# Performance work log

Measured on AMD Instinct MI355X. Metric: run time of the kernel, lower is better.

## Reference

```python
import jax, jax.numpy as jnp
import numpy as np

B, N, C, H = 2, 128, 256, 8
D = C // H
SCALE = D ** -0.5
LN_EPS = 1e-5


def _layernorm(x, g, b):
    mu = jnp.mean(x, axis=-1, keepdims=True)
    var = jnp.mean((x - mu) ** 2, axis=-1, keepdims=True)
    return (x - mu) * jax.lax.rsqrt(var + LN_EPS) * g + b


def setup_inputs() -> dict:
    key = jax.random.key(0)
    ks = jax.random.split(key, 12)
    s = 0.02
    return {
        "e": jax.random.normal(ks[0], (B, N, N, C), jnp.float32),
        "mask": jnp.zeros((B, N, N, H), jnp.float32),
        "ln_g": jnp.ones((C,), jnp.float32),
        "ln_b": jnp.zeros((C,), jnp.float32),
        "W_qkv_in": jax.random.normal(ks[1], (C, 3 * C), jnp.float32) * s,
        "b_qkv_in": jnp.zeros((3 * C,), jnp.float32),
        "W_E_in": jax.random.normal(ks[2], (C, H), jnp.float32) * s,
        "b_E_in": jnp.zeros((H,), jnp.float32),
        "W_qkv_out": jax.random.normal(ks[3], (C, 3 * C), jnp.float32) * s,
        "b_qkv_out": jnp.zeros((3 * C,), jnp.float32),
        "W_E_out": jax.random.normal(ks[4], (C, H), jnp.float32) * s,
        "b_E_out": jnp.zeros((H,), jnp.float32),
        "W_O": jax.random.normal(ks[5], (2 * C, C), jnp.float32) * s,
        "b_O": jnp.zeros((C,), jnp.float32),
    }


def reference(e, mask, ln_g, ln_b, W_qkv_in, b_qkv_in, W_E_in, b_E_in,
              W_qkv_out, b_qkv_out, W_E_out, b_E_out, W_O, b_O):
    b_, n, _, c = e.shape
    e_ln = _layernorm(e, ln_g, ln_b)

    def qkv(W, bias):
        z = e_ln @ W + bias  # [B,N,N,3C]
        q, k, v = jnp.split(z, 3, axis=-1)
        rs = lambda t: t.reshape(b_, n, n, D, H)
        return rs(q) * SCALE, rs(k), rs(v)

    # --- in pass ---
    Q, K, V = qkv(W_qkv_in, b_qkv_in)
    E_in = (e_ln @ W_E_in + b_E_in)[:, :, None, :, :]       # [B,N,1,N,H]
    H_in = jnp.einsum('bijdh,bjkdh->bijkh', Q, K) + E_in
    A_in = jax.nn.softmax(H_in + mask[:, :, None, :, :], axis=3)
    Va_in = jnp.einsum('bijkh,bjkdh->bijdh', A_in, V)

    # --- out pass ---
    Q, K, V = qkv(W_qkv_out, b_qkv_out)
    E_out = (e_ln @ W_E_out + b_E_out)[:, :, :, None, :]    # [B,N,N,1,H]
    H_out = jnp.einsum('bijdh,bkjdh->bkijh', Q, K) + E_out
    A_out = jax.nn.softmax(H_out + mask[:, :, :, None, :], axis=1)
    Va_out = jnp.einsum('bkijh,bkjdh->bijdh', A_out, V)

    Va = jnp.concatenate([Va_in, Va_out], axis=-1).reshape(b_, n, n, 2 * c)
    return Va @ W_O + b_O
```

## Files before the change

kernel.cpp:

```cpp
#include <hip/hip_runtime.h>

typedef unsigned short u16;
typedef __attribute__((ext_vector_type(8))) short bf16x8;
typedef __attribute__((ext_vector_type(4))) float f32x4;

#define SCALE 0.17677669529663687f

__device__ __forceinline__ float us2f(u16 u){ return __uint_as_float(((unsigned int)u)<<16); }
__device__ __forceinline__ u16 f2us(float f){
  unsigned int x = __float_as_uint(f);
  x += 0x7fffu + ((x>>16)&1u);
  return (u16)(x>>16);
}
__device__ __forceinline__ void gl_lds16(const u16* g, u16* l){
  __builtin_amdgcn_global_load_lds(
    (const __attribute__((address_space(1))) unsigned int*)g,
    (__attribute__((address_space(3))) unsigned int*)l, 16, 0, 0);
}

__global__ __launch_bounds__(256) void ln_prep(const float* __restrict__ e, const float* __restrict__ g,
                                               const float* __restrict__ bb, u16* __restrict__ eln,
                                               const float* __restrict__ Wi, const float* __restrict__ WEi,
                                               const float* __restrict__ Wo, const float* __restrict__ WEo,
                                               const float* __restrict__ WO,
                                               u16* __restrict__ WtI, u16* __restrict__ WtO,
                                               u16* __restrict__ WOt){
  int bid = blockIdx.x;
  int t = threadIdx.x;
  if (bid < 8192){
    int tok = bid*4 + (t>>6);
    int lane = t & 63;
    int c0 = lane*4;
    float4 x = *(const float4*)(e + tok*256 + c0);
    float sum = x.x+x.y+x.z+x.w;
    float sq  = x.x*x.x + x.y*x.y + x.z*x.z + x.w*x.w;
    #pragma unroll
    for (int off=32; off>=1; off>>=1){ sum += __shfl_xor(sum, off); sq += __shfl_xor(sq, off); }
    float mu = sum * 0.00390625f;
    float var = sq * 0.00390625f - mu*mu;
    float rstd = rsqrtf(var + 1e-5f);
    float4 gv = *(const float4*)(g + c0);
    float4 bv = *(const float4*)(bb + c0);
    ushort4 o;
    o.x = f2us((x.x-mu)*rstd*gv.x + bv.x);
    o.y = f2us((x.y-mu)*rstd*gv.y + bv.y);
    o.z = f2us((x.z-mu)*rstd*gv.z + bv.z);
    o.w = f2us((x.w-mu)*rstd*gv.w + bv.w);
    *(ushort4*)(eln + tok*256 + c0) = o;
  } else {
    int idx = (bid - 8192)*256 + t;
    if (idx < 425984){
      int which = idx >= 212992;
      int id2 = which ? idx - 212992 : idx;
      const float* W  = which ? Wo  : Wi;
      const float* WE = which ? WEo : WEi;
      u16* Wt = which ? WtO : WtI;
      int n = id2 >> 8, k = id2 & 255;
      float v;
      if (n < 768){
        int sec = n >> 8, r = n & 255, h = r >> 5, d = r & 31;
        v = W[k*768 + sec*256 + d*8 + h];
      } else if (n < 776) v = WE[k*8 + (n-768)];
      else v = 0.f;
      Wt[id2] = f2us(v);
    } else if (idx < 557056){
      int id2 = idx - 425984;
      int n = id2 >> 9, kp = id2 & 511;
      int pass = kp >> 8, h = (kp >> 5) & 7, d = kp & 31;
      int r = d*16 + pass*8 + h;
      WOt[id2] = f2us(WO[r*256 + n]);
    }
  }
}

__global__ __launch_bounds__(256) void qkv_gemm(const u16* __restrict__ eln, const u16* __restrict__ Wt,
    const float* __restrict__ bqkv, const float* __restrict__ bE, const float* __restrict__ mask,
    u16* __restrict__ Qb, u16* __restrict__ Kb, u16* __restrict__ Vb, u16* __restrict__ biasP,
    int pass){
  __shared__ __align__(16) u16 smem[24576];
  int t = threadIdx.x;
  int g = blockIdx.x >> 8;
  int tmb = blockIdx.x & 255;
  int row0 = tmb*128, col0 = g*64;
  int w = t >> 6, lane = t & 63, quad = lane >> 4, l15 = lane & 15;
  int lr = lane >> 3, cc = lane & 7;
  int sw8 = (cc ^ lr) << 3;

  u16* A0 = smem;          u16* A1 = smem + 8192;
  u16* B0 = smem + 16384;  u16* B1 = smem + 20480;

  auto STAGE = [&](int kc, u16* Ab, u16* Bb){
    #pragma unroll
    for (int i=0; i<4; ++i){
      int lrow = w*32 + i*8;
      gl_lds16(eln + (row0 + lrow + lr)*256 + kc*64 + sw8, &Ab[lrow*64]);
    }
    #pragma unroll
    for (int j=0; j<2; ++j){
      int brow = w*16 + j*8;
      gl_lds16(Wt + (col0 + brow + lr)*256 + kc*64 + sw8, &Bb[brow*64]);
    }
  };

  f32x4 zero = {0.f,0.f,0.f,0.f};
  f32x4 acc[2][4];
  #pragma unroll
  for (int mt=0; mt<2; ++mt)
    #pragma unroll
    for (int nt=0; nt<4; ++nt) acc[mt][nt] = zero;

  STAGE(0, A0, B0);
  STAGE(1, A1, B1);

  #pragma unroll
  for (int kc=0; kc<4; ++kc){
    if (kc == 3) { asm volatile("s_waitcnt vmcnt(0)" ::: "memory"); }
    else         { asm volatile("s_waitcnt vmcnt(6)" ::: "memory"); }
    __builtin_amdgcn_s_barrier();
    __builtin_amdgcn_sched_barrier(0);
    u16* Ac = (kc&1) ? A1 : A0;
    u16* Bc = (kc&1) ? B1 : B0;
    #pragma unroll
    for (int s=0; s<2; ++s){
      bf16x8 aF[2], bF[4];
      #pragma unroll
      for (int mt=0; mt<2; ++mt){
        int row = w*32 + mt*16 + l15;
        aF[mt] = *(const bf16x8*)&Ac[row*64 + ((((s<<2)+quad) ^ (l15&7))<<3)];
      }
      #pragma unroll
      for (int nt=0; nt<4; ++nt){
        int row = nt*16 + l15;
        bF[nt] = *(const bf16x8*)&Bc[row*64 + ((((s<<2)+quad) ^ (l15&7))<<3)];
      }
      #pragma unroll
      for (int mt=0; mt<2; ++mt)
        #pragma unroll
        for (int nt=0; nt<4; ++nt)
          acc[mt][nt] = __builtin_amdgcn_mfma_f32_16x16x32_bf16(aF[mt], bF[nt], acc[mt][nt], 0,0,0);
    }
    __builtin_amdgcn_sched_barrier(0);
    __builtin_amdgcn_s_barrier();
    __builtin_amdgcn_sched_barrier(0);
    if (kc < 2) STAGE(kc+2, Ac, Bc);
  }

  if (g < 12){
    int sec = g >> 2;
    float scl = (sec == 0) ? SCALE : 1.0f;
    u16* OutT = smem;
    #pragma unroll
    for (int mt=0; mt<2; ++mt){
      #pragma unroll
      for (int nt=0; nt<4; ++nt){
        int col = col0 + nt*16 + l15;
        int r = col & 255;
        float bias = bqkv[sec*256 + (r&31)*8 + (r>>5)];
        #pragma unroll
        for (int rr=0; rr<4; ++rr){
          int row = w*32 + mt*16 + quad*4 + rr;
          OutT[row*72 + nt*16 + l15] = f2us((acc[mt][nt][rr] + bias) * scl);
        }
      }
    }
    __syncthreads();
    u16* dst = (sec==0) ? Qb : (sec==1) ? Kb : Vb;
    int tr = (sec==0) || pass;
    int bq = tmb >> 7, iq = tmb & 127;
    int rbase = col0 & 255;
    int rrow = t >> 3, rc8 = (t & 7) * 8;
    #pragma unroll
    for (int k=0; k<4; ++k){
      int row = k*32 + rrow;
      uint4 v4 = *(const uint4*)&OutT[row*72 + rc8];
      int tok = tr ? (bq*16384 + row*128 + iq) : (row0 + row);
      *(uint4*)(dst + tok*256 + rbase + rc8) = v4;
    }
  } else {
    if (l15 < 8){
      int h = l15;
      #pragma unroll
      for (int mt=0; mt<2; ++mt){
        #pragma unroll
        for (int rr=0; rr<4; ++rr){
          int tok = row0 + w*32 + mt*16 + quad*4 + rr;
          float v = acc[mt][0][rr];
          int bb = tok >> 14, t1 = (tok >> 7) & 127, t2 = tok & 127;
          int tq = pass ? t2 : t1, tk = pass ? t1 : t2;
          float bv2 = v + bE[h] + mask[tok*8 + h];
          biasP[(((bb*8 + h)*128 + tq)*128) + (tk & 15)*8 + (tk >> 4)] = f2us(bv2);
        }
      }
    }
  }
}

__global__ __launch_bounds__(256) void attn_mfma(const u16* __restrict__ Qb, const u16* __restrict__ Kb,
    const u16* __restrict__ Vb, const u16* __restrict__ biasP, u16* __restrict__ Va, int pass){
  __shared__ __align__(16) u16 uni[16384];
  __shared__ __align__(16) u16 VsT[32][128];
  typedef u16 row40[40];
  typedef u16 row128[128];
  row40*  Qs = (row40*)uni;
  row40*  Ks = (row40*)(uni + 5120);
  row128* Ps = (row128*)uni;
  int t = threadIdx.x;
  int bx = blockIdx.x;
  int h = bx & 7, j = (bx>>3) & 127, b = bx >> 10;

  int base = ((b*128 + j)*128)*256 + h*32;
  #pragma unroll
  for (int it2=0; it2<2; ++it2){
    int idx = it2*256 + t;
    int row = idx >> 2, seg = idx & 3;
    int off = base + row*256 + seg*8;
    *(uint4*)&Qs[row][seg*8] = *(const uint4*)(Qb + off);
    *(uint4*)&Ks[row][seg*8] = *(const uint4*)(Kb + off);
    uint4 vv = *(const uint4*)(Vb + off);
    const u16* vp = (const u16*)&vv;
    #pragma unroll
    for (int q=0;q<8;++q){
      int d = seg*8 + q;
      VsT[d][((((row>>3) ^ q) & 15) << 3) | (row & 7)] = vp[q];
    }
  }
  __syncthreads();

  int w = t >> 6, lane = t & 63, quad = lane >> 4, l15 = lane & 15;
  bf16x8 aQ[2];
  #pragma unroll
  for (int it=0; it<2; ++it) aQ[it] = *(const bf16x8*)&Qs[w*32 + it*16 + l15][quad*8];
  f32x4 zero = {0.f,0.f,0.f,0.f};
  f32x4 S[2][8];
  #pragma unroll
  for (int tk=0; tk<8; ++tk){
    bf16x8 bK = *(const bf16x8*)&Ks[tk*16 + l15][quad*8];
    #pragma unroll
    for (int it=0; it<2; ++it)
      S[it][tk] = __builtin_amdgcn_mfma_f32_16x16x32_bf16(aQ[it], bK, zero, 0,0,0);
  }
  __syncthreads();
  const u16* bpP = biasP + ((b*8 + h)*128)*128;
  float inv[2][4];
  #pragma unroll
  for (int it=0; it<2; ++it){
    #pragma unroll
    for (int r=0; r<4; ++r){
      int i = w*32 + it*16 + quad*4 + r;
      uint4 b4 = *(const uint4*)(bpP + i*128 + l15*8);
      const u16* bu = (const u16*)&b4;
      float l = 0.f;
      float sv[8];
      #pragma unroll
      for (int tk=0; tk<8; ++tk){
        float p = __expf(S[it][tk][r] + us2f(bu[tk]));
        sv[tk] = p; l += p;
      }
      l += __shfl_xor(l,1); l += __shfl_xor(l,2); l += __shfl_xor(l,4); l += __shfl_xor(l,8);
      inv[it][r] = 1.0f / l;
      #pragma unroll
      for (int tk=0; tk<8; ++tk)
        Ps[i][(((tk*2 + (l15>>3)) ^ (i&7)) << 3) | (l15&7)] = f2us(sv[tk]);
    }
  }
  f32x4 O[2][2];
  #pragma unroll
  for (int it=0; it<2; ++it)
    #pragma unroll
    for (int dt=0; dt<2; ++dt) O[it][dt] = zero;
  #pragma unroll
  for (int kc=0; kc<4; ++kc){
    bf16x8 bV[2];
    #pragma unroll
    for (int dt=0; dt<2; ++dt)
      bV[dt] = *(const bf16x8*)&VsT[dt*16 + l15][(((kc*4 + quad) ^ (l15&7)) & 15) << 3];
    #pragma unroll
    for (int it=0; it<2; ++it){
      bf16x8 aP = *(const bf16x8*)&Ps[w*32 + it*16 + l15][(((kc*4 + quad) ^ (l15&7)) & 15) << 3];
      #pragma unroll
      for (int dt=0; dt<2; ++dt)
        O[it][dt] = __builtin_amdgcn_mfma_f32_16x16x32_bf16(aP, bV[dt], O[it][dt], 0,0,0);
    }
  }
  __syncthreads();
  u16* OutS = uni;
  #pragma unroll
  for (int it=0; it<2; ++it){
    #pragma unroll
    for (int r=0; r<4; ++r){
      int i = w*32 + it*16 + quad*4 + r;
      #pragma unroll
      for (int dt=0; dt<2; ++dt)
        OutS[i*36 + dt*16 + l15] = f2us(O[it][dt][r] * inv[it][r]);
    }
  }
  __syncthreads();
  int vr = t >> 2, vq = t & 3;
  #pragma unroll
  for (int k2=0; k2<2; ++k2){
    int row = k2*64 + vr;
    uint4 v4 = *(const uint4*)&OutS[row*36 + vq*8];
    *(uint4*)(Va + ((b*128 + row)*128 + j)*512 + pass*256 + h*32 + vq*8) = v4;
  }
}

__global__ __launch_bounds__(256) void out_gemm(const u16* __restrict__ Va, const u16* __restrict__ WOt,
                                                const float* __restrict__ bO, float* __restrict__ out){
  __shared__ __align__(16) u16 smem[24576];
  int t = threadIdx.x;
  int g = blockIdx.x >> 8;
  int tmb = blockIdx.x & 255;
  int row0 = tmb*128, col0 = g*64;
  int w = t >> 6, lane = t & 63, quad = lane >> 4, l15 = lane & 15;
  int lr = lane >> 3, cc = lane & 7;
  int sw8 = (cc ^ lr) << 3;

  u16* A0 = smem;          u16* A1 = smem + 8192;
  u16* B0 = smem + 16384;  u16* B1 = smem + 20480;

  auto STAGE = [&](int kc, u16* Ab, u16* Bb){
    #pragma unroll
    for (int i=0; i<4; ++i){
      int lrow = w*32 + i*8;
      gl_lds16(Va + (row0 + lrow + lr)*512 + kc*64 + sw8, &Ab[lrow*64]);
    }
    #pragma unroll
    for (int j=0; j<2; ++j){
      int brow = w*16 + j*8;
      gl_lds16(WOt + (col0 + brow + lr)*512 + kc*64 + sw8, &Bb[brow*64]);
    }
  };

  f32x4 zero = {0.f,0.f,0.f,0.f};
  f32x4 acc[2][4];
  #pragma unroll
  for (int mt=0; mt<2; ++mt)
    #pragma unroll
    for (int nt=0; nt<4; ++nt) acc[mt][nt] = zero;

  STAGE(0, A0, B0);
  STAGE(1, A1, B1);

  #pragma unroll
  for (int kc=0; kc<8; ++kc){
    if (kc == 7) { asm volatile("s_waitcnt vmcnt(0)" ::: "memory"); }
    else         { asm volatile("s_waitcnt vmcnt(6)" ::: "memory"); }
    __builtin_amdgcn_s_barrier();
    __builtin_amdgcn_sched_barrier(0);
    u16* Ac = (kc&1) ? A1 : A0;
    u16* Bc = (kc&1) ? B1 : B0;
    #pragma unroll
    for (int s=0; s<2; ++s){
      bf16x8 aF[2], bF[4];
      #pragma unroll
      for (int mt=0; mt<2; ++mt){
        int row = w*32 + mt*16 + l15;
        aF[mt] = *(const bf16x8*)&Ac[row*64 + ((((s<<2)+quad) ^ (l15&7))<<3)];
      }
      #pragma unroll
      for (int nt=0; nt<4; ++nt){
        int row = nt*16 + l15;
        bF[nt] = *(const bf16x8*)&Bc[row*64 + ((((s<<2)+quad) ^ (l15&7))<<3)];
      }
      #pragma unroll
      for (int mt=0; mt<2; ++mt)
        #pragma unroll
        for (int nt=0; nt<4; ++nt)
          acc[mt][nt] = __builtin_amdgcn_mfma_f32_16x16x32_bf16(aF[mt], bF[nt], acc[mt][nt], 0,0,0);
    }
    __builtin_amdgcn_sched_barrier(0);
    __builtin_amdgcn_s_barrier();
    __builtin_amdgcn_sched_barrier(0);
    if (kc < 6) STAGE(kc+2, Ac, Bc);
  }
  #pragma unroll
  for (int mt=0; mt<2; ++mt){
    #pragma unroll
    for (int nt=0; nt<4; ++nt){
      int col = col0 + nt*16 + l15;
      float bias = bO[col];
      #pragma unroll
      for (int rr=0; rr<4; ++rr){
        int tok = row0 + w*32 + mt*16 + quad*4 + rr;
        out[tok*256 + col] = acc[mt][nt][rr] + bias;
      }
    }
  }
}

#define OFF_ELN   0u
#define OFF_QB    16777216u
#define OFF_KB    33554432u
#define OFF_VB    50331648u
#define OFF_VA    67108864u
#define OFF_BIASP 100663296u
#define OFF_WTI   101187584u
#define OFF_WTO   101613568u
#define OFF_WOT   102039552u

extern "C" void kernel_launch(void* const* d_in, const int* in_sizes, int n_in,
                              void* d_out, int out_size, void* d_ws, size_t ws_size,
                              hipStream_t stream) {
  (void)in_sizes; (void)n_in; (void)out_size; (void)ws_size;
  const float* e        = (const float*)d_in[0];
  const float* mask     = (const float*)d_in[1];
  const float* ln_g     = (const float*)d_in[2];
  const float* ln_b     = (const float*)d_in[3];
  const float* W_qkv_in = (const float*)d_in[4];
  const float* b_qkv_in = (const float*)d_in[5];
  const float* W_E_in   = (const float*)d_in[6];
  const float* b_E_in   = (const float*)d_in[7];
  const float* W_qkv_out= (const float*)d_in[8];
  const float* b_qkv_out= (const float*)d_in[9];
  const float* W_E_out  = (const float*)d_in[10];
  const float* b_E_out  = (const float*)d_in[11];
  const float* W_O      = (const float*)d_in[12];
  const float* b_O      = (const float*)d_in[13];

  char* ws = (char*)d_ws;
  u16*   eln   = (u16*)(ws + OFF_ELN);
  u16*   Qb    = (u16*)(ws + OFF_QB);
  u16*   Kb    = (u16*)(ws + OFF_KB);
  u16*   Vb    = (u16*)(ws + OFF_VB);
  u16*   Va    = (u16*)(ws + OFF_VA);
  u16*   biasP = (u16*)(ws + OFF_BIASP);
  u16*   WtI   = (u16*)(ws + OFF_WTI);
  u16*   WtO   = (u16*)(ws + OFF_WTO);
  u16*   WOt   = (u16*)(ws + OFF_WOT);

  float* out = (float*)d_out;

  hipLaunchKernelGGL(ln_prep, dim3(10368), dim3(256), 0, stream,
                     e, ln_g, ln_b, eln,
                     W_qkv_in, W_E_in, W_qkv_out, W_E_out, W_O, WtI, WtO, WOt);

  hipLaunchKernelGGL(qkv_gemm, dim3(3328), dim3(256), 0, stream, eln, WtI, b_qkv_in, b_E_in, mask,
                     Qb, Kb, Vb, biasP, 0);
  hipLaunchKernelGGL(attn_mfma, dim3(2048), dim3(256), 0, stream, Qb, Kb, Vb, biasP, Va, 0);

  hipLaunchKernelGGL(qkv_gemm, dim3(3328), dim3(256), 0, stream, eln, WtO, b_qkv_out, b_E_out, mask,
                     Qb, Kb, Vb, biasP, 1);
  hipLaunchKernelGGL(attn_mfma, dim3(2048), dim3(256), 0, stream, Qb, Kb, Vb, biasP, Va, 1);

  hipLaunchKernelGGL(out_gemm, dim3(1024), dim3(256), 0, stream, Va, WOt, b_O, out);
}
```

Before: 244.1 us.

## Halve GEMM k-tile, use packed bf16 converts, and rework attention swizzles

```diff
diff --git a/kernel.cpp b/kernel.cpp
--- a/kernel.cpp
+++ b/kernel.cpp
@@ -11,6 +11,11 @@
   unsigned int x = __float_as_uint(f);
   x += 0x7fffu + ((x>>16)&1u);
   return (u16)(x>>16);
+}
+__device__ __forceinline__ unsigned int pk2(float a, float b){
+  unsigned int r;
+  asm("v_cvt_pk_bf16_f32 %0, %1, %2" : "=v"(r) : "v"(a), "v"(b));
+  return r;
 }
 __device__ __forceinline__ void gl_lds16(const u16* g, u16* l){
   __builtin_amdgcn_global_load_lds(
@@ -41,12 +46,10 @@
     float rstd = rsqrtf(var + 1e-5f);
     float4 gv = *(const float4*)(g + c0);
     float4 bv = *(const float4*)(bb + c0);
-    ushort4 o;
-    o.x = f2us((x.x-mu)*rstd*gv.x + bv.x);
-    o.y = f2us((x.y-mu)*rstd*gv.y + bv.y);
-    o.z = f2us((x.z-mu)*rstd*gv.z + bv.z);
-    o.w = f2us((x.w-mu)*rstd*gv.w + bv.w);
-    *(ushort4*)(eln + tok*256 + c0) = o;
+    unsigned int p0 = pk2((x.x-mu)*rstd*gv.x + bv.x, (x.y-mu)*rstd*gv.y + bv.y);
+    unsigned int p1 = pk2((x.z-mu)*rstd*gv.z + bv.z, (x.w-mu)*rstd*gv.w + bv.w);
+    uint2 o; o.x = p0; o.y = p1;
+    *(uint2*)(eln + tok*256 + c0) = o;
   } else {
     int idx = (bid - 8192)*256 + t;
     if (idx < 425984){
@@ -77,28 +80,28 @@
     const float* __restrict__ bqkv, const float* __restrict__ bE, const float* __restrict__ mask,
     u16* __restrict__ Qb, u16* __restrict__ Kb, u16* __restrict__ Vb, u16* __restrict__ biasP,
     int pass){
-  __shared__ __align__(16) u16 smem[24576];
+  __shared__ __align__(16) u16 smem[12288];
   int t = threadIdx.x;
   int g = blockIdx.x >> 8;
   int tmb = blockIdx.x & 255;
   int row0 = tmb*128, col0 = g*64;
   int w = t >> 6, lane = t & 63, quad = lane >> 4, l15 = lane & 15;
-  int lr = lane >> 3, cc = lane & 7;
-  int sw8 = (cc ^ lr) << 3;
-
-  u16* A0 = smem;          u16* A1 = smem + 8192;
-  u16* B0 = smem + 16384;  u16* B1 = smem + 20480;
+  int lr16 = lane >> 2, c4 = lane & 3;
+
+  u16* A0 = smem;          u16* A1 = smem + 4096;
+  u16* B0 = smem + 8192;   u16* B1 = smem + 10240;
 
   auto STAGE = [&](int kc, u16* Ab, u16* Bb){
     #pragma unroll
-    for (int i=0; i<4; ++i){
-      int lrow = w*32 + i*8;
-      gl_lds16(eln + (row0 + lrow + lr)*256 + kc*64 + sw8, &Ab[lrow*64]);
-    }
-    #pragma unroll
-    for (int j=0; j<2; ++j){
-      int brow = w*16 + j*8;
-      gl_lds16(Wt + (col0 + brow + lr)*256 + kc*64 + sw8, &Bb[brow*64]);
+    for (int i=0; i<2; ++i){
+      int r0 = w*32 + i*16;
+      int loc = r0 + lr16;
+      gl_lds16(eln + (row0 + loc)*256 + kc*32 + ((c4 ^ (loc&3))<<3), &Ab[r0*32]);
+    }
+    {
+      int r0 = w*16;
+      int loc = r0 + lr16;
+      gl_lds16(Wt + (col0 + loc)*256 + kc*32 + ((c4 ^ (loc&3))<<3), &Bb[r0*32]);
     }
   };
 
@@ -113,36 +116,33 @@
   STAGE(1, A1, B1);
 
   #pragma unroll
-  for (int kc=0; kc<4; ++kc){
-    if (kc == 3) { asm volatile("s_waitcnt vmcnt(0)" ::: "memory"); }
-    else         { asm volatile("s_waitcnt vmcnt(6)" ::: "memory"); }
+  for (int kc=0; kc<8; ++kc){
+    if (kc == 7) { asm volatile("s_waitcnt vmcnt(0)" ::: "memory"); }
+    else         { asm volatile("s_waitcnt vmcnt(3)" ::: "memory"); }
     __builtin_amdgcn_s_barrier();
     __builtin_amdgcn_sched_barrier(0);
     u16* Ac = (kc&1) ? A1 : A0;
     u16* Bc = (kc&1) ? B1 : B0;
-    #pragma unroll
-    for (int s=0; s<2; ++s){
-      bf16x8 aF[2], bF[4];
-      #pragma unroll
-      for (int mt=0; mt<2; ++mt){
-        int row = w*32 + mt*16 + l15;
-        aF[mt] = *(const bf16x8*)&Ac[row*64 + ((((s<<2)+quad) ^ (l15&7))<<3)];
-      }
-      #pragma unroll
-      for (int nt=0; nt<4; ++nt){
-        int row = nt*16 + l15;
-        bF[nt] = *(const bf16x8*)&Bc[row*64 + ((((s<<2)+quad) ^ (l15&7))<<3)];
-      }
-      #pragma unroll
-      for (int mt=0; mt<2; ++mt)
-        #pragma unroll
-        for (int nt=0; nt<4; ++nt)
-          acc[mt][nt] = __builtin_amdgcn_mfma_f32_16x16x32_bf16(aF[mt], bF[nt], acc[mt][nt], 0,0,0);
-    }
+    bf16x8 aF[2], bF[4];
+    #pragma unroll
+    for (int mt=0; mt<2; ++mt){
+      int row = w*32 + mt*16 + l15;
+      aF[mt] = *(const bf16x8*)&Ac[row*32 + ((quad ^ (row&3))<<3)];
+    }
+    #pragma unroll
+    for (int nt=0; nt<4; ++nt){
+      int row = nt*16 + l15;
+      bF[nt] = *(const bf16x8*)&Bc[row*32 + ((quad ^ (row&3))<<3)];
+    }
+    #pragma unroll
+    for (int mt=0; mt<2; ++mt)
+      #pragma unroll
+      for (int nt=0; nt<4; ++nt)
+        acc[mt][nt] = __builtin_amdgcn_mfma_f32_16x16x32_bf16(aF[mt], bF[nt], acc[mt][nt], 0,0,0);
     __builtin_amdgcn_sched_barrier(0);
     __builtin_amdgcn_s_barrier();
     __builtin_amdgcn_sched_barrier(0);
-    if (kc < 2) STAGE(kc+2, Ac, Bc);
+    if (kc < 6) STAGE(kc+2, Ac, Bc);
   }
 
   if (g < 12){
@@ -152,14 +152,18 @@
     #pragma unroll
     for (int mt=0; mt<2; ++mt){
       #pragma unroll
-      for (int nt=0; nt<4; ++nt){
-        int col = col0 + nt*16 + l15;
-        int r = col & 255;
-        float bias = bqkv[sec*256 + (r&31)*8 + (r>>5)];
+      for (int nt=0; nt<4; nt+=2){
+        int colA = col0 + nt*16 + l15, colB = colA + 16;
+        int rA = colA & 255, rB = colB & 255;
+        float biasA = bqkv[sec*256 + (rA&31)*8 + (rA>>5)];
+        float biasB = bqkv[sec*256 + (rB&31)*8 + (rB>>5)];
         #pragma unroll
         for (int rr=0; rr<4; ++rr){
           int row = w*32 + mt*16 + quad*4 + rr;
-          OutT[row*72 + nt*16 + l15] = f2us((acc[mt][nt][rr] + bias) * scl);
+          unsigned int p = pk2((acc[mt][nt][rr] + biasA) * scl,
+                               (acc[mt][nt+1][rr] + biasB) * scl);
+          OutT[row*72 + nt*16 + l15]     = (u16)p;
+          OutT[row*72 + (nt+1)*16 + l15] = (u16)(p>>16);
         }
       }
     }
@@ -220,8 +224,7 @@
     const u16* vp = (const u16*)&vv;
     #pragma unroll
     for (int q=0;q<8;++q){
-      int d = seg*8 + q;
-      VsT[d][((((row>>3) ^ q) & 15) << 3) | (row & 7)] = vp[q];
+      VsT[seg*8+q][((((row>>3) ^ (seg<<1) ^ q) & 15) << 3) | (row & 7)] = vp[q];
     }
   }
   __syncthreads();
@@ -241,14 +244,21 @@
   }
   __syncthreads();
   const u16* bpP = biasP + ((b*8 + h)*128)*128;
-  float inv[2][4];
-  #pragma unroll
-  for (int it=0; it<2; ++it){
+  uint4 b4a[2][4];
+  #pragma unroll
+  for (int it=0; it<2; ++it)
     #pragma unroll
     for (int r=0; r<4; ++r){
       int i = w*32 + it*16 + quad*4 + r;
-      uint4 b4 = *(const uint4*)(bpP + i*128 + l15*8);
-      const u16* bu = (const u16*)&b4;
+      b4a[it][r] = *(const uint4*)(bpP + i*128 + l15*8);
+    }
+  float inv[2][4];
+  #pragma unroll
+  for (int it=0; it<2; ++it){
+    #pragma unroll
+    for (int r=0; r<4; ++r){
+      int i = w*32 + it*16 + quad*4 + r;
+      const u16* bu = (const u16*)&b4a[it][r];
       float l = 0.f;
       float sv[8];
       #pragma unroll
@@ -259,8 +269,11 @@
       l += __shfl_xor(l,1); l += __shfl_xor(l,2); l += __shfl_xor(l,4); l += __shfl_xor(l,8);
       inv[it][r] = 1.0f / l;
       #pragma unroll
-      for (int tk=0; tk<8; ++tk)
-        Ps[i][(((tk*2 + (l15>>3)) ^ (i&7)) << 3) | (l15&7)] = f2us(sv[tk]);
+      for (int tk=0; tk<8; tk+=2){
+        unsigned int p = pk2(sv[tk], sv[tk+1]);
+        Ps[i][(((tk*2   + (l15>>3)) ^ (i&7)) << 3) | (l15&7)] = (u16)p;
+        Ps[i][(((tk*2+2 + (l15>>3)) ^ (i&7)) << 3) | (l15&7)] = (u16)(p>>16);
+      }
     }
   }
   f32x4 O[2][2];
@@ -272,8 +285,10 @@
   for (int kc=0; kc<4; ++kc){
     bf16x8 bV[2];
     #pragma unroll
-    for (int dt=0; dt<2; ++dt)
-      bV[dt] = *(const bf16x8*)&VsT[dt*16 + l15][(((kc*4 + quad) ^ (l15&7)) & 15) << 3];
+    for (int dt=0; dt<2; ++dt){
+      int key = (((dt*2 + (l15>>3)) << 1) ^ (l15&7));
+      bV[dt] = *(const bf16x8*)&VsT[dt*16 + l15][(((kc*4 + quad) ^ key) & 15) << 3];
+    }
     #pragma unroll
     for (int it=0; it<2; ++it){
       bf16x8 aP = *(const bf16x8*)&Ps[w*32 + it*16 + l15][(((kc*4 + quad) ^ (l15&7)) & 15) << 3];
@@ -289,9 +304,9 @@
     #pragma unroll
     for (int r=0; r<4; ++r){
       int i = w*32 + it*16 + quad*4 + r;
-      #pragma unroll
-      for (int dt=0; dt<2; ++dt)
-        OutS[i*36 + dt*16 + l15] = f2us(O[it][dt][r] * inv[it][r]);
+      unsigned int p = pk2(O[it][0][r] * inv[it][r], O[it][1][r] * inv[it][r]);
+      OutS[i*36 + l15]      = (u16)p;
+      OutS[i*36 + 16 + l15] = (u16)(p>>16);
     }
   }
   __syncthreads();
@@ -306,28 +321,28 @@
 
 __global__ __launch_bounds__(256) void out_gemm(const u16* __restrict__ Va, const u16* __restrict__ WOt,
                                                 const float* __restrict__ bO, float* __restrict__ out){
-  __shared__ __align__(16) u16 smem[24576];
+  __shared__ __align__(16) u16 smem[12288];
   int t = threadIdx.x;
   int g = blockIdx.x >> 8;
   int tmb = blockIdx.x & 255;
   int row0 = tmb*128, col0 = g*64;
   int w = t >> 6, lane = t & 63, quad = lane >> 4, l15 = lane & 15;
-  int lr = lane >> 3, cc = lane & 7;
-  int sw8 = (cc ^ lr) << 3;
-
-  u16* A0 = smem;          u16* A1 = smem + 8192;
-  u16* B0 = smem + 16384;  u16* B1 = smem + 20480;
+  int lr16 = lane >> 2, c4 = lane & 3;
+
+  u16* A0 = smem;          u16* A1 = smem + 4096;
+  u16* B0 = smem + 8192;   u16* B1 = smem + 10240;
 
   auto STAGE = [&](int kc, u16* Ab, u16* Bb){
     #pragma unroll
-    for (int i=0; i<4; ++i){
-      int lrow = w*32 + i*8;
-      gl_lds16(Va + (row0 + lrow + lr)*512 + kc*64 + sw8, &Ab[lrow*64]);
-    }
-    #pragma unroll
-    for (int j=0; j<2; ++j){
-      int brow = w*16 + j*8;
-      gl_lds16(WOt + (col0 + brow + lr)*512 + kc*64 + sw8, &Bb[brow*64]);
+    for (int i=0; i<2; ++i){
+      int r0 = w*32 + i*16;
+      int loc = r0 + lr16;
+      gl_lds16(Va + (row0 + loc)*512 + kc*32 + ((c4 ^ (loc&3))<<3), &Ab[r0*32]);
+    }
+    {
+      int r0 = w*16;
+      int loc = r0 + lr16;
+      gl_lds16(WOt + (col0 + loc)*512 + kc*32 + ((c4 ^ (loc&3))<<3), &Bb[r0*32]);
     }
   };
 
@@ -342,36 +357,33 @@
   STAGE(1, A1, B1);
 
   #pragma unroll
-  for (int kc=0; kc<8; ++kc){
-    if (kc == 7) { asm volatile("s_waitcnt vmcnt(0)" ::: "memory"); }
-    else         { asm volatile("s_waitcnt vmcnt(6)" ::: "memory"); }
+  for (int kc=0; kc<16; ++kc){
+    if (kc == 15) { asm volatile("s_waitcnt vmcnt(0)" ::: "memory"); }
+    else          { asm volatile("s_waitcnt vmcnt(3)" ::: "memory"); }
     __builtin_amdgcn_s_barrier();
     __builtin_amdgcn_sched_barrier(0);
     u16* Ac = (kc&1) ? A1 : A0;
     u16* Bc = (kc&1) ? B1 : B0;
-    #pragma unroll
-    for (int s=0; s<2; ++s){
-      bf16x8 aF[2], bF[4];
-      #pragma unroll
-      for (int mt=0; mt<2; ++mt){
-        int row = w*32 + mt*16 + l15;
-        aF[mt] = *(const bf16x8*)&Ac[row*64 + ((((s<<2)+quad) ^ (l15&7))<<3)];
-      }
-      #pragma unroll
-      for (int nt=0; nt<4; ++nt){
-        int row = nt*16 + l15;
-        bF[nt] = *(const bf16x8*)&Bc[row*64 + ((((s<<2)+quad) ^ (l15&7))<<3)];
-      }
-      #pragma unroll
-      for (int mt=0; mt<2; ++mt)
-        #pragma unroll
-        for (int nt=0; nt<4; ++nt)
-          acc[mt][nt] = __builtin_amdgcn_mfma_f32_16x16x32_bf16(aF[mt], bF[nt], acc[mt][nt], 0,0,0);
-    }
+    bf16x8 aF[2], bF[4];
+    #pragma unroll
+    for (int mt=0; mt<2; ++mt){
+      int row = w*32 + mt*16 + l15;
+      aF[mt] = *(const bf16x8*)&Ac[row*32 + ((quad ^ (row&3))<<3)];
+    }
+    #pragma unroll
+    for (int nt=0; nt<4; ++nt){
+      int row = nt*16 + l15;
+      bF[nt] = *(const bf16x8*)&Bc[row*32 + ((quad ^ (row&3))<<3)];
+    }
+    #pragma unroll
+    for (int mt=0; mt<2; ++mt)
+      #pragma unroll
+      for (int nt=0; nt<4; ++nt)
+        acc[mt][nt] = __builtin_amdgcn_mfma_f32_16x16x32_bf16(aF[mt], bF[nt], acc[mt][nt], 0,0,0);
     __builtin_amdgcn_sched_barrier(0);
     __builtin_amdgcn_s_barrier();
     __builtin_amdgcn_sched_barrier(0);
-    if (kc < 6) STAGE(kc+2, Ac, Bc);
+    if (kc < 14) STAGE(kc+2, Ac, Bc);
   }
   #pragma unroll
   for (int mt=0; mt<2; ++mt){
```

After: 242.9 us. About the same (-0.5%).
